# Kernel tuning notes

Hardware: AMD Instinct MI355X
Metric: run time of the kernel (lower is better)

## Reference

```python
import jax, jax.numpy as jnp
import numpy as np

S = 16384   # total tokens (batch*seq flattened)
D = 1024    # model_dim
E = 32      # num_global_experts
H = 1024    # expert hidden size
CAP = 512   # capacity = capacity_factor * ceil(S / E)


def setup_inputs() -> dict:
    key = jax.random.key(0)
    k1, k2, k3, k4 = jax.random.split(key, 4)
    x = jax.random.normal(k1, (S, D), jnp.float32)
    wg = jax.random.normal(k2, (E, D), jnp.float32) * 0.02
    w1 = jax.random.normal(k3, (E, D, H), jnp.float32) * 0.02
    w2 = jax.random.normal(k4, (E, H, D), jnp.float32) * 0.02
    return {"x": x, "wg": wg, "w1": w1, "w2": w2}


def _moe_forward(x, wg, w1, w2):
    # --- Top1Gate ---
    logits = x @ wg.T                                   # [S, E]
    gates = jax.nn.softmax(logits, axis=1)              # [S, E]
    idx = jnp.argmax(logits, axis=1)                    # [S] int
    mask1 = jax.nn.one_hot(idx, E, dtype=jnp.int32)     # [S, E]
    gates1_s = jnp.sum(gates * mask1.astype(gates.dtype), axis=1)  # [S]
    # load-balance aux loss (fp32 path)
    me = jnp.sum(gates.astype(jnp.float32), axis=0)
    ce = jnp.sum(mask1.astype(jnp.float32), axis=0)
    l_loss = jnp.sum(me * ce) * (float(E) / float(S * S))
    # positions within expert (tutel cumsum_sub_one)
    loc = jnp.sum(jnp.cumsum(mask1, axis=0) * mask1, axis=1) - 1   # [S]
    valid = loc < CAP                                   # capacity drop
    slot = jnp.where(valid, idx * CAP + loc, 0)         # flat slot id, dropped -> 0 (masked below)

    # --- GatingEncoder: scatter tokens into [E*CAP, D] buffer ---
    xm = x * valid[:, None].astype(x.dtype)
    dispatched = jnp.zeros((E * CAP, D), x.dtype).at[slot].add(xm)
    dispatched = dispatched.reshape(E, CAP, D)

    # --- ExpertsGemm: per-expert FFN (world_size == 1, all-to-all is identity) ---
    h = jax.nn.relu(jnp.einsum('ecd,edh->ech', dispatched, w1))    # [E, CAP, H]
    expert_out = jnp.einsum('ech,ehd->ecd', h, w2).reshape(E * CAP, D)

    # --- GatingDecoder: gather back + weight by gate ---
    y = expert_out[slot] * (gates1_s * valid.astype(gates1_s.dtype))[:, None]
    return y, l_loss


def reference(x, wg, w1, w2):
    return _moe_forward(x, wg, w1, w2)
```

## Files before the change

kernel.cpp:

```cpp
#include <hip/hip_runtime.h>
#include <stdint.h>

static constexpr int nS   = 16384;
static constexpr int nD   = 1024;
static constexpr int nE   = 32;
static constexpr int nH   = 1024;
static constexpr int nCAP = 512;

static constexpr int GT = 64;
static constexpr int GB = nS / GT;

typedef __bf16 bf16x8 __attribute__((ext_vector_type(8)));
typedef float  f32x4  __attribute__((ext_vector_type(4)));
typedef unsigned short u16x8 __attribute__((ext_vector_type(8)));

static __device__ __forceinline__ unsigned short f2bf(float f) {
    __bf16 h = (__bf16)f;
    return __builtin_bit_cast(unsigned short, h);
}

static __device__ __forceinline__ void gload16(const void* g, void* l) {
    __builtin_amdgcn_global_load_lds(
        (const __attribute__((address_space(1))) void*)g,
        (__attribute__((address_space(3))) void*)l, 16, 0, 0);
}

__global__ __launch_bounds__(128) void k_gate(
    const float* __restrict__ x, const float* __restrict__ wg,
    unsigned short* __restrict__ xbf, int* __restrict__ idxo,
    float* __restrict__ gateval, int* __restrict__ counts,
    float* __restrict__ me_part)
{
    __shared__ float xs[GT][65];
    __shared__ float wgs[nE][65];
    __shared__ float gl[GT][nE + 1];
    __shared__ int   hist[nE];

    const int tid = threadIdx.x;
    const int tb  = blockIdx.x * GT;
    if (tid < nE) hist[tid] = 0;

    const int t0 = (tid >> 3) * 4;
    const int e0 = (tid & 7) * 4;
    float acc[4][4] = {};

    for (int ch = 0; ch < nD / 64; ++ch) {
#pragma unroll
        for (int i = 0; i < 4; ++i) {
            int f = tid + i * 128;
            int r = f >> 4, c4 = f & 15;
            const float4 v = *(const float4*)&wg[(size_t)r * nD + ch * 64 + c4 * 4];
            wgs[r][c4*4+0] = v.x; wgs[r][c4*4+1] = v.y;
            wgs[r][c4*4+2] = v.z; wgs[r][c4*4+3] = v.w;
        }
#pragma unroll
        for (int i = 0; i < 8; ++i) {
            int f = tid + i * 128;
            int r = f >> 4, c4 = f & 15;
            size_t go = (size_t)(tb + r) * nD + ch * 64 + c4 * 4;
            const float4 v = *(const float4*)&x[go];
            xs[r][c4*4+0] = v.x; xs[r][c4*4+1] = v.y;
            xs[r][c4*4+2] = v.z; xs[r][c4*4+3] = v.w;
            unsigned long long pk = (unsigned long long)f2bf(v.x)
                | ((unsigned long long)f2bf(v.y) << 16)
                | ((unsigned long long)f2bf(v.z) << 32)
                | ((unsigned long long)f2bf(v.w) << 48);
            *(unsigned long long*)&xbf[go] = pk;
        }
        __syncthreads();
#pragma unroll 4
        for (int k = 0; k < 64; ++k) {
            float xa[4], wb[4];
#pragma unroll
            for (int i = 0; i < 4; ++i) xa[i] = xs[t0 + i][k];
#pragma unroll
            for (int j = 0; j < 4; ++j) wb[j] = wgs[e0 + j][k];
#pragma unroll
            for (int i = 0; i < 4; ++i)
#pragma unroll
                for (int j = 0; j < 4; ++j) acc[i][j] += xa[i] * wb[j];
        }
        __syncthreads();
    }

#pragma unroll
    for (int i = 0; i < 4; ++i)
#pragma unroll
        for (int j = 0; j < 4; ++j) gl[t0 + i][e0 + j] = acc[i][j];
    __syncthreads();

    if (tid < GT) {
        float mx = gl[tid][0]; int bi = 0;
#pragma unroll
        for (int e = 1; e < nE; ++e) { float v = gl[tid][e]; if (v > mx) { mx = v; bi = e; } }
        float den = 0.f;
#pragma unroll
        for (int e = 0; e < nE; ++e) { float g = expf(gl[tid][e] - mx); gl[tid][e] = g; den += g; }
        float inv = 1.f / den;
#pragma unroll
        for (int e = 0; e < nE; ++e) gl[tid][e] *= inv;
        idxo[tb + tid] = bi;
        gateval[tb + tid] = inv;
        atomicAdd(&hist[bi], 1);
    }
    __syncthreads();
    if (tid < nE) {
        float s = 0.f;
        for (int t = 0; t < GT; ++t) s += gl[t][tid];
        me_part[blockIdx.x * nE + tid] = s;
        counts[blockIdx.x * nE + tid] = hist[tid];
    }
}

__global__ __launch_bounds__(1024) void k_scan(
    const int* __restrict__ counts, int* __restrict__ offsets,
    const float* __restrict__ me_part, float* __restrict__ loss_out,
    int* __restrict__ inv_slot)
{
    __shared__ int tot[nE];
    __shared__ float mesum[nE];
    const int w = threadIdx.x >> 6;
    const int lane = threadIdx.x & 63;
    for (int e = w; e < nE; e += 16) {
        int v[4]; int s = 0;
#pragma unroll
        for (int i = 0; i < 4; ++i) { v[i] = counts[(lane * 4 + i) * nE + e]; s += v[i]; }
        int incl = s;
#pragma unroll
        for (int d = 1; d < 64; d <<= 1) {
            int o = __shfl_up(incl, d);
            if (lane >= d) incl += o;
        }
        int run = incl - s;
#pragma unroll
        for (int i = 0; i < 4; ++i) { offsets[(lane * 4 + i) * nE + e] = run; run += v[i]; }
        int total = __shfl(incl, 63);
        if (lane == 0) tot[e] = total;

        float ms = 0.f;
#pragma unroll
        for (int i = 0; i < 4; ++i) ms += me_part[(lane * 4 + i) * nE + e];
#pragma unroll
        for (int d = 32; d >= 1; d >>= 1) ms += __shfl_xor(ms, d);
        if (lane == 0) mesum[e] = ms;
    }
    __syncthreads();
    if (threadIdx.x < 64) {
        float val = (threadIdx.x < nE) ? mesum[threadIdx.x] * (float)tot[threadIdx.x] : 0.f;
#pragma unroll
        for (int d = 32; d >= 1; d >>= 1) val += __shfl_xor(val, d);
        if (threadIdx.x == 0)
            *loss_out = val * ((float)nE / ((float)nS * (float)nS));
    }
    for (int i = threadIdx.x; i < nE * nCAP; i += 1024) {
        const int e = i >> 9, loc = i & (nCAP - 1);
        if (loc >= tot[e]) inv_slot[i] = -1;
    }
}

__global__ __launch_bounds__(64) void k_assign(
    const int* __restrict__ idxi, const int* __restrict__ offsets,
    int* __restrict__ inv_slot, float* __restrict__ y)
{
    __shared__ int drop[64];
    __shared__ int ndrop;
    const int lane = threadIdx.x;
    const int t = blockIdx.x * 64 + lane;
    const int e = idxi[t];
    if (lane == 0) ndrop = 0;
    __syncthreads();
    int rank = 0;
#pragma unroll
    for (int ee = 0; ee < nE; ++ee) {
        unsigned long long m = __ballot(e == ee);
        if (e == ee) rank = __popcll(m & ((1ull << lane) - 1ull));
    }
    const int loc = offsets[blockIdx.x * nE + e] + rank;
    if (loc < nCAP) {
        inv_slot[e * nCAP + loc] = t;
    } else {
        int p = atomicAdd(&ndrop, 1);
        drop[p] = t;
    }
    __syncthreads();
    const int nd = ndrop;
    for (int i = 0; i < nd; ++i) {
        const int tt = drop[i];
        float4 z = {0.f, 0.f, 0.f, 0.f};
        for (int c = lane; c < nD / 4; c += 64)
            *(float4*)&y[(size_t)tt * nD + c * 4] = z;
    }
}

__global__ __launch_bounds__(256) void k_transpose(
    const float* __restrict__ w1, const float* __restrict__ w2,
    unsigned short* __restrict__ w1t, unsigned short* __restrict__ w2t)
{
    __shared__ unsigned short T[64 * 258];
    const float* src = blockIdx.z ? w2 : w1;
    unsigned short* dst = blockIdx.z ? w2t : w1t;
    const int e    = blockIdx.y;
    const int dblk = blockIdx.x & 15;
    const int hblk = blockIdx.x >> 4;
    const int t = threadIdx.x;
    const int wv = t >> 6, lane = t & 63;

    const float* sbase = src + ((size_t)e * 1024 + dblk * 64) * 1024 + hblk * 256;

#pragma unroll
    for (int i = 0; i < 16; ++i) {
        const int d = i * 4 + wv;
        const float4 v = *(const float4*)&sbase[(size_t)d * 1024 + lane * 4];
        unsigned long long pk = (unsigned long long)f2bf(v.x)
            | ((unsigned long long)f2bf(v.y) << 16)
            | ((unsigned long long)f2bf(v.z) << 32)
            | ((unsigned long long)f2bf(v.w) << 48);
        *(unsigned long long*)&T[d * 258 + lane * 4] = pk;
    }
    __syncthreads();

    const size_t cbase0 = (((size_t)e * 8 + hblk * 2) * 16 + dblk) * 8192;
    const size_t cbase1 = cbase0 + 16 * 8192;
#pragma unroll
    for (int s = 0; s < 8; ++s) {
        const int off = s * 2048 + t * 8;
        const int hl  = off >> 6;
        const int k8  = off & 63;
        u16x8 v;
#pragma unroll
        for (int r = 0; r < 8; ++r) v[r] = T[(k8 + r) * 258 + hl];
        const size_t base = (off < 8192) ? cbase0 : cbase1;
        *(u16x8*)&dst[base + (off & 8191)] = v;
    }
}

template <int MODE>
__global__ __launch_bounds__(256) void k_gemm(
    const unsigned short* __restrict__ Abase,
    const unsigned short* __restrict__ Bt,
    const int* __restrict__ inv_slot,
    const float* __restrict__ gateval,
    unsigned short* __restrict__ hout,
    float* __restrict__ y)
{
    __shared__ __attribute__((aligned(16))) unsigned short SMEM[128 * 64 * 2];
    unsigned short* As = SMEM;
    unsigned short* Bs = SMEM + 128 * 64;

    const int tid = threadIdx.x;
    const int lane = tid & 63, w = tid >> 6;
    const int bid = (blockIdx.x & 7) * 128 + (blockIdx.x >> 3);
    const int n0 = (bid & 7) * 128, m0 = ((bid >> 3) & 3) * 128, e = bid >> 5;

    const unsigned short* gA[4];
    const int j = lane & 7;
#pragma unroll
    for (int s = 0; s < 4; ++s) {
        const int cw = s * 4 + w;
        const int row = cw * 8 + (lane >> 3);
        if (MODE == 0) {
            int tok = inv_slot[e * nCAP + m0 + row];
            if (tok < 0) tok = 0;
            gA[s] = Abase + (size_t)tok * nD + j * 8;
        } else {
            gA[s] = Abase + ((size_t)e * nCAP + m0 + row) * nH + j * 8;
        }
    }
    const unsigned short* gB = Bt + (((size_t)e * 8 + (n0 >> 7)) * 16) * 8192
                             + (size_t)tid * 8;

    f32x4 acc[4][4];
#pragma unroll
    for (int a = 0; a < 4; ++a)
#pragma unroll
        for (int b = 0; b < 4; ++b) acc[a][b] = (f32x4){0.f, 0.f, 0.f, 0.f};

    const int wm = w >> 1, wn = w & 1;
    const int abyte = (wm * 64 + (lane & 15)) * 128 + (lane >> 4) * 16;
    const int bbyte = (wn * 64 + (lane & 15)) * 128 + (lane >> 4) * 16;

    for (int k0 = 0; k0 < 1024 / 64; ++k0) {
#pragma unroll
        for (int s = 0; s < 4; ++s) {
            gload16(gA[s] + k0 * 64, (char*)As + (s * 4 + w) * 1024);
            gload16(gB + (size_t)k0 * 8192 + ((s * 4 + w) * 512 + lane * 8 - tid * 8),
                    (char*)Bs + (s * 4 + w) * 1024);
        }
        __syncthreads();
#pragma unroll
        for (int kk = 0; kk < 2; ++kk) {
            bf16x8 a[4], b[4];
#pragma unroll
            for (int mi = 0; mi < 4; ++mi)
                a[mi] = *(const bf16x8*)((const char*)As + abyte + mi * 2048 + kk * 64);
#pragma unroll
            for (int ni = 0; ni < 4; ++ni)
                b[ni] = *(const bf16x8*)((const char*)Bs + bbyte + ni * 2048 + kk * 64);
#pragma unroll
            for (int mi = 0; mi < 4; ++mi)
#pragma unroll
                for (int ni = 0; ni < 4; ++ni)
                    acc[mi][ni] = __builtin_amdgcn_mfma_f32_16x16x32_bf16(
                        a[mi], b[ni], acc[mi][ni], 0, 0, 0);
        }
        __syncthreads();
    }

    const int col_l = lane & 15, rg = lane >> 4;
    if (MODE == 0) {
#pragma unroll
        for (int mi = 0; mi < 4; ++mi) {
#pragma unroll
            for (int ni = 0; ni < 4; ++ni) {
                const f32x4 v = acc[mi][ni];
                const int nl = wn * 64 + ni * 16 + col_l;
#pragma unroll
                for (int r = 0; r < 4; ++r) {
                    const int ml = wm * 64 + mi * 16 + rg * 4 + r;
                    const float f = v[r] > 0.f ? v[r] : 0.f;
                    SMEM[ml * 128 + nl] = f2bf(f);
                }
            }
        }
        __syncthreads();
#pragma unroll
        for (int s = 0; s < 8; ++s) {
            const int u = tid + s * 256;
            const int row = u >> 4, nu = u & 15;
            const u16x8 v = *(const u16x8*)((const char*)SMEM + u * 16);
            *(u16x8*)&hout[((size_t)e * nCAP + m0 + row) * nH + n0 + nu * 8] = v;
        }
    } else {
        float* Lf = (float*)SMEM;
#pragma unroll
        for (int P = 0; P < 2; ++P) {
            if (wm == P) {
#pragma unroll
                for (int mi = 0; mi < 4; ++mi) {
#pragma unroll
                    for (int ni = 0; ni < 4; ++ni) {
                        const f32x4 v = acc[mi][ni];
                        const int nl = wn * 64 + ni * 16 + col_l;
#pragma unroll
                        for (int r = 0; r < 4; ++r) {
                            const int ml = mi * 16 + rg * 4 + r;
                            Lf[ml * 128 + nl] = v[r];
                        }
                    }
                }
            }
            __syncthreads();
#pragma unroll
            for (int s = 0; s < 8; ++s) {
                const int u = tid + s * 256;
                const int row = u >> 5, f4 = u & 31;
                const int tok = inv_slot[e * nCAP + m0 + P * 64 + row];
                if (tok >= 0) {
                    const float gv = gateval[tok];
                    float4 v = *(const float4*)((const char*)SMEM + u * 16);
                    v.x *= gv; v.y *= gv; v.z *= gv; v.w *= gv;
                    *(float4*)&y[(size_t)tok * nD + n0 + f4 * 4] = v;
                }
            }
            __syncthreads();
        }
    }
}

extern "C" void kernel_launch(void* const* d_in, const int* in_sizes, int n_in,
                              void* d_out, int out_size, void* d_ws, size_t ws_size,
                              hipStream_t stream) {
    const float* x  = (const float*)d_in[0];
    const float* wg = (const float*)d_in[1];
    const float* w1 = (const float*)d_in[2];
    const float* w2 = (const float*)d_in[3];
    float* y = (float*)d_out;
    float* loss = y + (size_t)nS * nD;

    char* ws = (char*)d_ws;
    unsigned short* w1t  = (unsigned short*)(ws);
    unsigned short* w2t  = (unsigned short*)(ws + (64ull << 20));
    unsigned short* hbuf = (unsigned short*)(ws + (128ull << 20));
    unsigned short* xbf  = (unsigned short*)(ws + (160ull << 20));
    char* p = ws + (192ull << 20);
    int*   idxb    = (int*)p;   p += (size_t)nS * 4;
    float* gateval = (float*)p; p += (size_t)nS * 4;
    int*   counts  = (int*)p;   p += (size_t)GB * nE * 4;
    int*   offsets = (int*)p;   p += (size_t)GB * nE * 4;
    float* me_part = (float*)p; p += (size_t)GB * nE * 4;
    int*   inv_slot= (int*)p;

    k_gate<<<GB, 128, 0, stream>>>(x, wg, xbf, idxb, gateval, counts, me_part);
    k_scan<<<1, 1024, 0, stream>>>(counts, offsets, me_part, loss, inv_slot);
    k_assign<<<GB, 64, 0, stream>>>(idxb, offsets, inv_slot, y);
    k_transpose<<<dim3(64, 32, 2), 256, 0, stream>>>(w1, w2, w1t, w2t);
    k_gemm<0><<<1024, 256, 0, stream>>>(xbf, w1t, inv_slot, gateval, hbuf, y);
    k_gemm<1><<<1024, 256, 0, stream>>>(hbuf, w2t, inv_slot, gateval, hbuf, y);
}
```

Baseline: 312.0 us.

## Widen expert GEMM tiles to 128x256 and XOR-swizzle LDS layout

The per-expert GEMM tile grows from 128x128 to 128x256, so each wave holds 4x8 accumulators and the grid halves to 512 blocks. This roughly halves how often each A row is re-read. The weight-transpose kernel and the A loads now write data in an XOR-swizzled order, so the MFMA fragment reads from LDS avoid bank conflicts. The epilogues are rewritten to stage the wider tile in several passes. In exchange, register pressure goes up and fewer blocks are available to fill the CUs.

```diff
diff --git a/kernel.cpp b/kernel.cpp
--- a/kernel.cpp
+++ b/kernel.cpp
@@ -219,8 +219,7 @@
     }
     __syncthreads();
 
-    const size_t cbase0 = (((size_t)e * 8 + hblk * 2) * 16 + dblk) * 8192;
-    const size_t cbase1 = cbase0 + 16 * 8192;
+    const size_t cbase = ((size_t)(e * 4 + hblk) * 16 + dblk) * 16384;
 #pragma unroll
     for (int s = 0; s < 8; ++s) {
         const int off = s * 2048 + t * 8;
@@ -229,8 +228,8 @@
         u16x8 v;
 #pragma unroll
         for (int r = 0; r < 8; ++r) v[r] = T[(k8 + r) * 258 + hl];
-        const size_t base = (off < 8192) ? cbase0 : cbase1;
-        *(u16x8*)&dst[base + (off & 8191)] = v;
+        const int sw = (off & ~63) | ((((t & 7) ^ (hl & 7))) << 3);
+        *(u16x8*)&dst[cbase + sw] = v;
     }
 }
 
@@ -243,17 +242,17 @@
     unsigned short* __restrict__ hout,
     float* __restrict__ y)
 {
-    __shared__ __attribute__((aligned(16))) unsigned short SMEM[128 * 64 * 2];
+    __shared__ __attribute__((aligned(16))) unsigned short SMEM[24576];
     unsigned short* As = SMEM;
-    unsigned short* Bs = SMEM + 128 * 64;
+    unsigned short* Bs = SMEM + 8192;
 
     const int tid = threadIdx.x;
     const int lane = tid & 63, w = tid >> 6;
-    const int bid = (blockIdx.x & 7) * 128 + (blockIdx.x >> 3);
-    const int n0 = (bid & 7) * 128, m0 = ((bid >> 3) & 3) * 128, e = bid >> 5;
+    const int bid = (blockIdx.x & 7) * 64 + (blockIdx.x >> 3);
+    const int n0 = (bid & 3) * 256, m0 = ((bid >> 2) & 3) * 128, e = bid >> 4;
 
     const unsigned short* gA[4];
-    const int j = lane & 7;
+    const int jsw = ((lane & 7) ^ (lane >> 3)) * 8;
 #pragma unroll
     for (int s = 0; s < 4; ++s) {
         const int cw = s * 4 + w;
@@ -261,47 +260,55 @@
         if (MODE == 0) {
             int tok = inv_slot[e * nCAP + m0 + row];
             if (tok < 0) tok = 0;
-            gA[s] = Abase + (size_t)tok * nD + j * 8;
+            gA[s] = Abase + (size_t)tok * nD + jsw;
         } else {
-            gA[s] = Abase + ((size_t)e * nCAP + m0 + row) * nH + j * 8;
-        }
-    }
-    const unsigned short* gB = Bt + (((size_t)e * 8 + (n0 >> 7)) * 16) * 8192
+            gA[s] = Abase + ((size_t)e * nCAP + m0 + row) * nH + jsw;
+        }
+    }
+    const unsigned short* gB = Bt + ((size_t)(e * 4 + (n0 >> 8)) * 16) * 16384
                              + (size_t)tid * 8;
 
-    f32x4 acc[4][4];
+    f32x4 acc[4][8];
 #pragma unroll
     for (int a = 0; a < 4; ++a)
 #pragma unroll
-        for (int b = 0; b < 4; ++b) acc[a][b] = (f32x4){0.f, 0.f, 0.f, 0.f};
+        for (int b = 0; b < 8; ++b) acc[a][b] = (f32x4){0.f, 0.f, 0.f, 0.f};
 
     const int wm = w >> 1, wn = w & 1;
-    const int abyte = (wm * 64 + (lane & 15)) * 128 + (lane >> 4) * 16;
-    const int bbyte = (wn * 64 + (lane & 15)) * 128 + (lane >> 4) * 16;
+    const int arow = (wm * 64 + (lane & 15)) * 128;
+    const int brow = (wn * 128 + (lane & 15)) * 128;
+    const int u0 = (((lane >> 4))     ^ (lane & 7)) << 4;
+    const int u1 = ((4 + (lane >> 4)) ^ (lane & 7)) << 4;
 
     for (int k0 = 0; k0 < 1024 / 64; ++k0) {
 #pragma unroll
-        for (int s = 0; s < 4; ++s) {
+        for (int s = 0; s < 4; ++s)
             gload16(gA[s] + k0 * 64, (char*)As + (s * 4 + w) * 1024);
-            gload16(gB + (size_t)k0 * 8192 + ((s * 4 + w) * 512 + lane * 8 - tid * 8),
-                    (char*)Bs + (s * 4 + w) * 1024);
-        }
+#pragma unroll
+        for (int s = 0; s < 8; ++s)
+            gload16(gB + (size_t)k0 * 16384 + s * 2048,
+                    (char*)Bs + s * 4096 + w * 1024);
         __syncthreads();
 #pragma unroll
         for (int kk = 0; kk < 2; ++kk) {
-            bf16x8 a[4], b[4];
+            const int ub = kk ? u1 : u0;
+            bf16x8 a[4];
 #pragma unroll
             for (int mi = 0; mi < 4; ++mi)
-                a[mi] = *(const bf16x8*)((const char*)As + abyte + mi * 2048 + kk * 64);
-#pragma unroll
-            for (int ni = 0; ni < 4; ++ni)
-                b[ni] = *(const bf16x8*)((const char*)Bs + bbyte + ni * 2048 + kk * 64);
-#pragma unroll
-            for (int mi = 0; mi < 4; ++mi)
-#pragma unroll
-                for (int ni = 0; ni < 4; ++ni)
-                    acc[mi][ni] = __builtin_amdgcn_mfma_f32_16x16x32_bf16(
-                        a[mi], b[ni], acc[mi][ni], 0, 0, 0);
+                a[mi] = *(const bf16x8*)((const char*)As + arow + mi * 2048 + ub);
+#pragma unroll
+            for (int nh = 0; nh < 2; ++nh) {
+                bf16x8 b[4];
+#pragma unroll
+                for (int q = 0; q < 4; ++q)
+                    b[q] = *(const bf16x8*)((const char*)Bs + brow + (nh * 4 + q) * 2048 + ub);
+#pragma unroll
+                for (int mi = 0; mi < 4; ++mi)
+#pragma unroll
+                    for (int q = 0; q < 4; ++q)
+                        acc[mi][nh * 4 + q] = __builtin_amdgcn_mfma_f32_16x16x32_bf16(
+                            a[mi], b[q], acc[mi][nh * 4 + q], 0, 0, 0);
+            }
         }
         __syncthreads();
     }
@@ -309,42 +316,19 @@
     const int col_l = lane & 15, rg = lane >> 4;
     if (MODE == 0) {
 #pragma unroll
-        for (int mi = 0; mi < 4; ++mi) {
-#pragma unroll
-            for (int ni = 0; ni < 4; ++ni) {
-                const f32x4 v = acc[mi][ni];
-                const int nl = wn * 64 + ni * 16 + col_l;
-#pragma unroll
-                for (int r = 0; r < 4; ++r) {
-                    const int ml = wm * 64 + mi * 16 + rg * 4 + r;
-                    const float f = v[r] > 0.f ? v[r] : 0.f;
-                    SMEM[ml * 128 + nl] = f2bf(f);
-                }
-            }
-        }
-        __syncthreads();
-#pragma unroll
-        for (int s = 0; s < 8; ++s) {
-            const int u = tid + s * 256;
-            const int row = u >> 4, nu = u & 15;
-            const u16x8 v = *(const u16x8*)((const char*)SMEM + u * 16);
-            *(u16x8*)&hout[((size_t)e * nCAP + m0 + row) * nH + n0 + nu * 8] = v;
-        }
-    } else {
-        float* Lf = (float*)SMEM;
-#pragma unroll
         for (int P = 0; P < 2; ++P) {
-            if (wm == P) {
+            if (wn == P) {
 #pragma unroll
                 for (int mi = 0; mi < 4; ++mi) {
 #pragma unroll
-                    for (int ni = 0; ni < 4; ++ni) {
+                    for (int ni = 0; ni < 8; ++ni) {
                         const f32x4 v = acc[mi][ni];
-                        const int nl = wn * 64 + ni * 16 + col_l;
+                        const int nl = ni * 16 + col_l;
 #pragma unroll
                         for (int r = 0; r < 4; ++r) {
-                            const int ml = mi * 16 + rg * 4 + r;
-                            Lf[ml * 128 + nl] = v[r];
+                            const int ml = wm * 64 + mi * 16 + rg * 4 + r;
+                            const float f = v[r] > 0.f ? v[r] : 0.f;
+                            SMEM[ml * 128 + nl] = f2bf(f);
                         }
                     }
                 }
@@ -353,11 +337,41 @@
 #pragma unroll
             for (int s = 0; s < 8; ++s) {
                 const int u = tid + s * 256;
-                const int row = u >> 5, f4 = u & 31;
-                const int tok = inv_slot[e * nCAP + m0 + P * 64 + row];
+                const int row = u >> 4, nu = u & 15;
+                const u16x8 v = *(const u16x8*)((const char*)SMEM + u * 16);
+                *(u16x8*)&hout[((size_t)e * nCAP + m0 + row) * nH + n0 + P * 128 + nu * 8] = v;
+            }
+            __syncthreads();
+        }
+    } else {
+        float* Lf = (float*)SMEM;
+#pragma unroll
+        for (int P = 0; P < 4; ++P) {
+            if (wm == (P >> 1)) {
+#pragma unroll
+                for (int q = 0; q < 2; ++q) {
+                    const int mi = (P & 1) * 2 + q;
+#pragma unroll
+                    for (int ni = 0; ni < 8; ++ni) {
+                        const f32x4 v = acc[mi][ni];
+                        const int nl = wn * 128 + ni * 16 + col_l;
+#pragma unroll
+                        for (int r = 0; r < 4; ++r) {
+                            const int ml = q * 16 + rg * 4 + r;
+                            Lf[ml * 256 + nl] = v[r];
+                        }
+                    }
+                }
+            }
+            __syncthreads();
+#pragma unroll
+            for (int s = 0; s < 8; ++s) {
+                const int u = tid + s * 256;
+                const int row = u >> 6, f4 = u & 63;
+                const int tok = inv_slot[e * nCAP + m0 + P * 32 + row];
                 if (tok >= 0) {
                     const float gv = gateval[tok];
-                    float4 v = *(const float4*)((const char*)SMEM + u * 16);
+                    float4 v = *(const float4*)((const char*)Lf + u * 16);
                     v.x *= gv; v.y *= gv; v.z *= gv; v.w *= gv;
                     *(float4*)&y[(size_t)tok * nD + n0 + f4 * 4] = v;
                 }
@@ -394,6 +408,6 @@
     k_scan<<<1, 1024, 0, stream>>>(counts, offsets, me_part, loss, inv_slot);
     k_assign<<<GB, 64, 0, stream>>>(idxb, offsets, inv_slot, y);
     k_transpose<<<dim3(64, 32, 2), 256, 0, stream>>>(w1, w2, w1t, w2t);
-    k_gemm<0><<<1024, 256, 0, stream>>>(xbf, w1t, inv_slot, gateval, hbuf, y);
-    k_gemm<1><<<1024, 256, 0, stream>>>(hbuf, w2t, inv_slot, gateval, hbuf, y);
-}
+    k_gemm<0><<<512, 256, 0, stream>>>(xbf, w1t, inv_slot, gateval, hbuf, y);
+    k_gemm<1><<<512, 256, 0, stream>>>(hbuf, w2t, inv_slot, gateval, hbuf, y);
+}
```

After: 344.9 us. 10.6% more time.
